# Performance work log

Measured on AMD Instinct MI355X. Metric: run time of the kernel, lower is better.

Reference implementation:

```python
import jax, jax.numpy as jnp
import numpy as np

N_NODES = 50000
N_EDGES = 800000


def setup_inputs() -> dict:
    key = jax.random.key(0)
    k_h, k_e, k_w1, k_w2 = jax.random.split(key, 4)
    d_in, d_hid, d_out = 128, 128, 128
    h = jax.random.normal(k_h, (N_NODES, d_in), dtype=jnp.float32)
    edge_index = jax.random.randint(k_e, (2, N_EDGES), 0, N_NODES, dtype=jnp.int64)
    # Linear weights ~ PyTorch default scale
    W1 = jax.random.normal(k_w1, (d_hid, d_in), dtype=jnp.float32) * (1.0 / np.sqrt(d_in))
    b1 = jnp.zeros((d_hid,), dtype=jnp.float32)
    W2 = jax.random.normal(k_w2, (d_out, d_hid), dtype=jnp.float32) * (1.0 / np.sqrt(d_hid))
    b2 = jnp.zeros((d_out,), dtype=jnp.float32)
    return {"h": h, "edge_index": edge_index, "W1": W1, "b1": b1, "W2": W2, "b2": b2}


def _sage_gcn(h, src, dst, W, b):
    # DGL SAGEConv with 'gcn' aggregator (eval mode):
    #   h_neigh = (segment_sum(h[src] -> dst) + h) / (in_deg + 1)
    #   out     = h_neigh @ W^T + b   (only fc_neigh is used for 'gcn')
    n = h.shape[0]
    agg = jax.ops.segment_sum(h[src], dst, num_segments=n)          # [N, d]
    deg = jax.ops.segment_sum(jnp.ones_like(dst, dtype=h.dtype), dst, num_segments=n)  # [N]
    h_neigh = (agg + h) / (deg[:, None] + 1.0)
    return h_neigh @ W.T + b


def reference(h, edge_index, W1, b1, W2, b2):
    src, dst = edge_index[0], edge_index[1]
    # Layer 1 + ReLU (dropout inactive in eval mode)
    h1 = jax.nn.relu(_sage_gcn(h, src, dst, W1, b1))
    # Layer 2 (no activation on final layer)
    return _sage_gcn(h1, src, dst, W2, b2)
```

## Files before the change

kernel.cpp:

```cpp
#include <hip/hip_runtime.h>

typedef unsigned short ushort_t;
typedef __attribute__((ext_vector_type(8))) short short8;
typedef __attribute__((ext_vector_type(8))) unsigned short ushort8;
typedef __attribute__((ext_vector_type(8))) __bf16 bf16x8;
typedef __attribute__((ext_vector_type(4))) float f32x4;

#define N_NODES 50000
#define N_EDGES 800000
#define D 128
#define N4 (N_NODES / 4)
#define BSTRIDE 64

#define XB_B    0
#define XB1_B   12800000
#define WBHI1_B 25600000
#define WBLO1_B 25632768
#define WBHI2_B 25665536
#define WBLO2_B 25698304
#define CNT_B   25731072
#define CSR_B   25931072

__device__ __forceinline__ ushort_t f2bf(float f) {
    unsigned u = __builtin_bit_cast(unsigned, f);
    return (ushort_t)((u + 0x7FFFu + ((u >> 16) & 1u)) >> 16);
}
__device__ __forceinline__ float bf2f(ushort_t b) {
    return __builtin_bit_cast(float, ((unsigned)b) << 16);
}

__device__ __forceinline__ f32x4 mfma16(short8 a, short8 b, f32x4 c) {
    return __builtin_amdgcn_mfma_f32_16x16x32_bf16(
        __builtin_bit_cast(bf16x8, a), __builtin_bit_cast(bf16x8, b), c, 0, 0, 0);
}

__device__ __forceinline__ int wfrag_off(int k, int j) {
    int nt = j >> 4;
    int kt = k >> 5;
    int lane = (((k >> 3) & 3) << 4) | (j & 15);
    int i = k & 7;
    return ((nt * 4 + kt) << 9) + (lane << 3) + i;
}

__global__ __launch_bounds__(256) void init_kernel(const float* __restrict__ h,
                                                   const float* __restrict__ W1,
                                                   const float* __restrict__ W2,
                                                   ushort_t* __restrict__ wbhi1,
                                                   ushort_t* __restrict__ wblo1,
                                                   ushort_t* __restrict__ wbhi2,
                                                   ushort_t* __restrict__ wblo2,
                                                   ushort_t* __restrict__ xb,
                                                   int* __restrict__ cnt) {
    int idx = blockIdx.x * 256 + threadIdx.x;
    if (idx < N4) {
        ((int4*)cnt)[idx] = make_int4(0, 0, 0, 0);
        return;
    }
    int i = idx - N4;
    if (i < D * D) {
        int j = i >> 7;
        int k = i & 127;
        int off = wfrag_off(k, j);
        float w1 = W1[i];
        ushort_t h1 = f2bf(w1);
        wbhi1[off] = h1;
        wblo1[off] = f2bf(w1 - bf2f(h1));
        float w2 = W2[i];
        ushort_t h2 = f2bf(w2);
        wbhi2[off] = h2;
        wblo2[off] = f2bf(w2 - bf2f(h2));
        return;
    }
    int j = i - D * D;
    if (j < N_NODES * D / 4) {
        float4 v = ((const float4*)h)[j];
        ushort4 o;
        o.x = f2bf(v.x); o.y = f2bf(v.y); o.z = f2bf(v.z); o.w = f2bf(v.w);
        ((ushort4*)xb)[j] = o;
    }
}

__global__ __launch_bounds__(256) void bucket_kernel(const int* __restrict__ src,
                                                     const int* __restrict__ dst,
                                                     int* __restrict__ cnt,
                                                     ushort_t* __restrict__ csr) {
    int e = blockIdx.x * 256 + threadIdx.x;
    if (e < N_EDGES) {
        int d = dst[e];
        int p = atomicAdd(&cnt[d], 1);
        if (p < BSTRIDE) csr[(size_t)d * BSTRIDE + p] = (ushort_t)src[e];
    }
}

template <int RELU, int OUTBF16>
__global__ __launch_bounds__(256, 6) void sage_fused_kernel(const ushort_t* __restrict__ xb,
                                                            const int* __restrict__ cnt,
                                                            const ushort_t* __restrict__ csr,
                                                            const ushort_t* __restrict__ wbhi,
                                                            const ushort_t* __restrict__ wblo,
                                                            const float* __restrict__ bias,
                                                            void* __restrict__ outp) {
    __shared__ ushort_t xl[32 * 136];
    const int t = threadIdx.x;
    const int n0 = blockIdx.x * 32;
    const int gg = t >> 4;
    const int cl = t & 15;
    const ushort8* xb8 = (const ushort8*)xb;

#pragma unroll
    for (int q = 0; q < 2; ++q) {
        int n = gg * 2 + q;
        int node = n0 + n;
        float acc[8];
        if (node < N_NODES) {
            ushort8 sv = xb8[(size_t)node * 16 + cl];
#pragma unroll
            for (int j = 0; j < 8; ++j) acc[j] = bf2f(sv[j]);
            int deg = cnt[node];
            if (deg > BSTRIDE) deg = BSTRIDE;
            const ushort_t* row = csr + (size_t)node * BSTRIDE;
            int i = 0;
            for (; i + 8 <= deg; i += 8) {
                ushort8 v[8];
#pragma unroll
                for (int u = 0; u < 8; ++u) {
                    int s = (int)row[i + u];
                    v[u] = xb8[(size_t)s * 16 + cl];
                }
#pragma unroll
                for (int u = 0; u < 8; ++u) {
#pragma unroll
                    for (int j = 0; j < 8; ++j) acc[j] += bf2f(v[u][j]);
                }
            }
            if (i + 4 <= deg) {
                ushort8 v[4];
#pragma unroll
                for (int u = 0; u < 4; ++u) {
                    int s = (int)row[i + u];
                    v[u] = xb8[(size_t)s * 16 + cl];
                }
#pragma unroll
                for (int u = 0; u < 4; ++u) {
#pragma unroll
                    for (int j = 0; j < 8; ++j) acc[j] += bf2f(v[u][j]);
                }
                i += 4;
            }
            for (; i < deg; ++i) {
                int s = (int)row[i];
                ushort8 v = xb8[(size_t)s * 16 + cl];
#pragma unroll
                for (int j = 0; j < 8; ++j) acc[j] += bf2f(v[j]);
            }
            float iv = 1.0f / (float)(deg + 1);
#pragma unroll
            for (int j = 0; j < 8; ++j) acc[j] *= iv;
        } else {
#pragma unroll
            for (int j = 0; j < 8; ++j) acc[j] = 0.f;
        }
        ushort8 o;
#pragma unroll
        for (int j = 0; j < 8; ++j) o[j] = f2bf(acc[j]);
        *(ushort8*)(&xl[n * 136 + cl * 8]) = o;
    }

    __syncthreads();

    const int w = t >> 6;
    const int l = t & 63;
    const int lr = l & 15;
    const int lg = l >> 4;
    const short8* bh = (const short8*)wbhi;
    const short8* bl = (const short8*)wblo;

    float b0 = bias[(2 * w) * 16 + lr];
    float b1 = bias[(2 * w + 1) * 16 + lr];
    f32x4 acc[2][2];
    acc[0][0] = (f32x4){b0, b0, b0, b0};
    acc[1][0] = (f32x4){b0, b0, b0, b0};
    acc[0][1] = (f32x4){b1, b1, b1, b1};
    acc[1][1] = (f32x4){b1, b1, b1, b1};

#pragma unroll
    for (int kt = 0; kt < 4; ++kt) {
        short8 a0 = *(const short8*)(&xl[lr * 136 + kt * 32 + lg * 8]);
        short8 a1 = *(const short8*)(&xl[(16 + lr) * 136 + kt * 32 + lg * 8]);
        short8 b0h = bh[((2 * w) * 4 + kt) * 64 + l];
        short8 b0l = bl[((2 * w) * 4 + kt) * 64 + l];
        short8 b1h = bh[((2 * w + 1) * 4 + kt) * 64 + l];
        short8 b1l = bl[((2 * w + 1) * 4 + kt) * 64 + l];
        acc[0][0] = mfma16(a0, b0h, acc[0][0]);
        acc[0][0] = mfma16(a0, b0l, acc[0][0]);
        acc[1][0] = mfma16(a1, b0h, acc[1][0]);
        acc[1][0] = mfma16(a1, b0l, acc[1][0]);
        acc[0][1] = mfma16(a0, b1h, acc[0][1]);
        acc[0][1] = mfma16(a0, b1l, acc[0][1]);
        acc[1][1] = mfma16(a1, b1h, acc[1][1]);
        acc[1][1] = mfma16(a1, b1l, acc[1][1]);
    }

#pragma unroll
    for (int mt = 0; mt < 2; ++mt) {
#pragma unroll
        for (int nn = 0; nn < 2; ++nn) {
            int col = (2 * w + nn) * 16 + lr;
#pragma unroll
            for (int r = 0; r < 4; ++r) {
                int node = n0 + mt * 16 + lg * 4 + r;
                if (node >= N_NODES) continue;
                float v = acc[mt][nn][r];
                if (RELU) v = fmaxf(v, 0.f);
                if (OUTBF16) {
                    ((ushort_t*)outp)[(size_t)node * 128 + col] = f2bf(v);
                } else {
                    ((float*)outp)[(size_t)node * 128 + col] = v;
                }
            }
        }
    }
}

extern "C" void kernel_launch(void* const* d_in, const int* in_sizes, int n_in,
                              void* d_out, int out_size, void* d_ws, size_t ws_size,
                              hipStream_t stream) {
    const float* h  = (const float*)d_in[0];
    const int*   ei = (const int*)d_in[1];
    const float* W1 = (const float*)d_in[2];
    const float* b1 = (const float*)d_in[3];
    const float* W2 = (const float*)d_in[4];
    const float* b2 = (const float*)d_in[5];
    char* ws = (char*)d_ws;

    ushort_t* xb    = (ushort_t*)(ws + XB_B);
    ushort_t* xb1   = (ushort_t*)(ws + XB1_B);
    ushort_t* wbhi1 = (ushort_t*)(ws + WBHI1_B);
    ushort_t* wblo1 = (ushort_t*)(ws + WBLO1_B);
    ushort_t* wbhi2 = (ushort_t*)(ws + WBHI2_B);
    ushort_t* wblo2 = (ushort_t*)(ws + WBLO2_B);
    int* cnt        = (int*)(ws + CNT_B);
    ushort_t* csr   = (ushort_t*)(ws + CSR_B);

    const int* src = ei;
    const int* dst = ei + N_EDGES;

    int init_threads = N4 + D * D + N_NODES * D / 4;
    init_kernel<<<(init_threads + 255) / 256, 256, 0, stream>>>(h, W1, W2, wbhi1, wblo1, wbhi2, wblo2, xb, cnt);
    bucket_kernel<<<(N_EDGES + 255) / 256, 256, 0, stream>>>(src, dst, cnt, csr);

    sage_fused_kernel<1, 1><<<(N_NODES + 31) / 32, 256, 0, stream>>>(xb, cnt, csr, wbhi1, wblo1, b1, (void*)xb1);
    sage_fused_kernel<0, 0><<<(N_NODES + 31) / 32, 256, 0, stream>>>(xb1, cnt, csr, wbhi2, wblo2, b2, d_out);
}
```

Measured before the change: 125.9 us.

## Pre-bin edges by destination range before CSR scatter for atomic locality

Replaces the single-pass atomic bucketing with two passes. The first pass partitions edges into 8 bins by destination range, using shared-memory counters and packed src/dst words. The second pass scatters each bin into the per-node CSR, so atomics and writes hit a narrower address range and get better cache locality. This adds an extra pass over the edges and a staging buffer aliased onto the layer-1 output workspace. Bins are capped, so a heavily skewed destination distribution would silently drop edges.

```diff
diff --git a/kernel.cpp b/kernel.cpp
--- a/kernel.cpp
+++ b/kernel.cpp
@@ -11,6 +11,11 @@
 #define D 128
 #define N4 (N_NODES / 4)
 #define BSTRIDE 64
+#define NBIN 8
+#define BIN_DIV 6250
+#define BIN_CAP 112640
+#define BIN_BLOCKS ((N_EDGES + 1023) / 1024)
+#define SC_BPB ((BIN_CAP + 255) / 256)
 
 #define XB_B    0
 #define XB1_B   12800000
@@ -19,7 +24,7 @@
 #define WBHI2_B 25665536
 #define WBLO2_B 25698304
 #define CNT_B   25731072
-#define CSR_B   25931072
+#define CSR_B   25931104
 
 __device__ __forceinline__ ushort_t f2bf(float f) {
     unsigned u = __builtin_bit_cast(unsigned, f);
@@ -52,11 +57,11 @@
                                                    ushort_t* __restrict__ xb,
                                                    int* __restrict__ cnt) {
     int idx = blockIdx.x * 256 + threadIdx.x;
-    if (idx < N4) {
+    if (idx < N4 + 2) {
         ((int4*)cnt)[idx] = make_int4(0, 0, 0, 0);
         return;
     }
-    int i = idx - N4;
+    int i = idx - (N4 + 2);
     if (i < D * D) {
         int j = i >> 7;
         int k = i & 127;
@@ -80,15 +85,58 @@
     }
 }
 
-__global__ __launch_bounds__(256) void bucket_kernel(const int* __restrict__ src,
-                                                     const int* __restrict__ dst,
-                                                     int* __restrict__ cnt,
-                                                     ushort_t* __restrict__ csr) {
-    int e = blockIdx.x * 256 + threadIdx.x;
-    if (e < N_EDGES) {
-        int d = dst[e];
+__global__ __launch_bounds__(256) void bin_kernel(const int* __restrict__ src,
+                                                  const int* __restrict__ dst,
+                                                  int* __restrict__ bincur,
+                                                  unsigned* __restrict__ binbuf) {
+    __shared__ int cnts[NBIN];
+    __shared__ int base[NBIN];
+    int t = threadIdx.x;
+    if (t < NBIN) cnts[t] = 0;
+    __syncthreads();
+    unsigned pk[4];
+    int bn[4];
+    int ofs[4];
+    int e0 = blockIdx.x * 1024 + t;
+#pragma unroll
+    for (int i = 0; i < 4; ++i) {
+        int e = e0 + i * 256;
+        bn[i] = -1;
+        if (e < N_EDGES) {
+            int s = src[e];
+            int d = dst[e];
+            pk[i] = (unsigned)s | ((unsigned)d << 16);
+            bn[i] = d / BIN_DIV;
+            ofs[i] = atomicAdd(&cnts[bn[i]], 1);
+        }
+    }
+    __syncthreads();
+    if (t < NBIN) base[t] = atomicAdd(&bincur[t], cnts[t]);
+    __syncthreads();
+#pragma unroll
+    for (int i = 0; i < 4; ++i) {
+        if (bn[i] >= 0) {
+            int pos = base[bn[i]] + ofs[i];
+            if (pos < BIN_CAP) binbuf[(size_t)bn[i] * BIN_CAP + pos] = pk[i];
+        }
+    }
+}
+
+__global__ __launch_bounds__(256) void scatter2_kernel(const unsigned* __restrict__ binbuf,
+                                                       const int* __restrict__ bincur,
+                                                       int* __restrict__ cnt,
+                                                       ushort_t* __restrict__ csr) {
+    int bin = blockIdx.x & 7;
+    int chunk = blockIdx.x >> 3;
+    int n = bincur[bin];
+    if (n > BIN_CAP) n = BIN_CAP;
+    int i = chunk * 256 + threadIdx.x;
+    if (i < n) {
+        unsigned pk = binbuf[(size_t)bin * BIN_CAP + i];
+        int s = (int)(pk & 0xFFFFu);
+        int d = (int)(pk >> 16);
         int p = atomicAdd(&cnt[d], 1);
-        if (p < BSTRIDE) csr[(size_t)d * BSTRIDE + p] = (ushort_t)src[e];
+        if (p < BSTRIDE) csr[(size_t)d * BSTRIDE + p] = (ushort_t)s;
     }
 }
 
@@ -235,19 +283,22 @@
 
     ushort_t* xb    = (ushort_t*)(ws + XB_B);
     ushort_t* xb1   = (ushort_t*)(ws + XB1_B);
+    unsigned* binbuf = (unsigned*)(ws + XB1_B);
     ushort_t* wbhi1 = (ushort_t*)(ws + WBHI1_B);
     ushort_t* wblo1 = (ushort_t*)(ws + WBLO1_B);
     ushort_t* wbhi2 = (ushort_t*)(ws + WBHI2_B);
     ushort_t* wblo2 = (ushort_t*)(ws + WBLO2_B);
     int* cnt        = (int*)(ws + CNT_B);
+    int* bincur     = cnt + N_NODES;
     ushort_t* csr   = (ushort_t*)(ws + CSR_B);
 
     const int* src = ei;
     const int* dst = ei + N_EDGES;
 
-    int init_threads = N4 + D * D + N_NODES * D / 4;
+    int init_threads = (N4 + 2) + D * D + N_NODES * D / 4;
     init_kernel<<<(init_threads + 255) / 256, 256, 0, stream>>>(h, W1, W2, wbhi1, wblo1, wbhi2, wblo2, xb, cnt);
-    bucket_kernel<<<(N_EDGES + 255) / 256, 256, 0, stream>>>(src, dst, cnt, csr);
+    bin_kernel<<<BIN_BLOCKS, 256, 0, stream>>>(src, dst, bincur, binbuf);
+    scatter2_kernel<<<NBIN * SC_BPB, 256, 0, stream>>>(binbuf, bincur, cnt, csr);
 
     sage_fused_kernel<1, 1><<<(N_NODES + 31) / 32, 256, 0, stream>>>(xb, cnt, csr, wbhi1, wblo1, b1, (void*)xb1);
     sage_fused_kernel<0, 0><<<(N_NODES + 31) / 32, 256, 0, stream>>>(xb1, cnt, csr, wbhi2, wblo2, b2, d_out);
```

Result: no change. 127.1 us (+1.0%).
